# Optimization experiments

Hardware: AMD Instinct MI355X
Metric: run time of the kernel (lower is better)

Reference implementation:

```python
import jax, jax.numpy as jnp
import numpy as np

OUT_H, OUT_W = 14, 14
SPATIAL_SCALE = 0.25

def setup_inputs() -> dict:
    key = jax.random.key(0)
    k1, k2, k3, k4, k5, k6 = jax.random.split(key, 6)
    B, C, H, W = 2, 256, 200, 336
    R = 1000
    features = jax.random.normal(k1, (B, C, H, W), jnp.float32)
    img_h, img_w = H / SPATIAL_SCALE, W / SPATIAL_SCALE
    cx = jax.random.uniform(k2, (R,)) * img_w
    cy = jax.random.uniform(k3, (R,)) * img_h
    bw = jax.random.uniform(k4, (R,)) * 256.0 + 16.0
    bh = jax.random.uniform(k5, (R,)) * 256.0 + 16.0
    x1 = jnp.clip(cx - bw / 2, 0.0, img_w - 1.0)
    x2 = jnp.clip(cx + bw / 2, 0.0, img_w - 1.0)
    y1 = jnp.clip(cy - bh / 2, 0.0, img_h - 1.0)
    y2 = jnp.clip(cy + bh / 2, 0.0, img_h - 1.0)
    bidx = jax.random.randint(k6, (R,), 0, B).astype(jnp.float32)
    rois = jnp.stack([bidx, x1, y1, x2, y2], axis=1)  # (R, 5)
    return {"features": features, "rois": rois}

def _roi_align(features, rois):
    # features: (B, C, H, W); rois: (R, 5) = (batch_idx, x1, y1, x2, y2) in image coords
    B, C, H, W = features.shape
    R = rois.shape[0]
    b = jax.lax.stop_gradient(rois[:, 0]).astype(jnp.int32)
    x1, y1, x2, y2 = rois[:, 1], rois[:, 2], rois[:, 3], rois[:, 4]
    # bin-center grid in [0,1] (affine_grid identity, align_corners=False, then normalized)
    gx = (jnp.arange(OUT_W, dtype=features.dtype) + 0.5) / OUT_W
    gy = (jnp.arange(OUT_H, dtype=features.dtype) + 0.5) / OUT_H
    px = x1[:, None] + gx[None, :] * (x2 - x1)[:, None]  # (R, OUT_W) abs image x
    py = y1[:, None] + gy[None, :] * (y2 - y1)[:, None]  # (R, OUT_H) abs image y
    # grid_sample(align_corners=False) with normalized coord abs/(size/scale): pix = abs*scale - 0.5
    fx = jnp.broadcast_to(px[:, None, :], (R, OUT_H, OUT_W)) * SPATIAL_SCALE - 0.5
    fy = jnp.broadcast_to(py[:, :, None], (R, OUT_H, OUT_W)) * SPATIAL_SCALE - 0.5
    x0 = jnp.floor(fx); y0 = jnp.floor(fy)
    lx = fx - x0; ly = fy - y0
    x0i = x0.astype(jnp.int32); y0i = y0.astype(jnp.int32)
    feats_flat = features.reshape(B, C, H * W)
    bb = b[:, None, None]  # (R,1,1)
    def corner(yi, xi):
        valid = ((xi >= 0) & (xi < W) & (yi >= 0) & (yi < H)).astype(features.dtype)
        idx = jnp.clip(yi, 0, H - 1) * W + jnp.clip(xi, 0, W - 1)  # (R,OUT_H,OUT_W)
        v = feats_flat[bb, :, idx]  # (R, OUT_H, OUT_W, C)
        return v * valid[..., None]  # zeros padding_mode
    v00 = corner(y0i, x0i)
    v01 = corner(y0i, x0i + 1)
    v10 = corner(y0i + 1, x0i)
    v11 = corner(y0i + 1, x0i + 1)
    wx0 = (1.0 - lx)[..., None]; wx1 = lx[..., None]
    wy0 = (1.0 - ly)[..., None]; wy1 = ly[..., None]
    out = wy0 * (wx0 * v00 + wx1 * v01) + wy1 * (wx0 * v10 + wx1 * v11)
    return out.transpose(0, 3, 1, 2)  # (R, C, OUT_H, OUT_W)

def reference(features, rois):
    return _roi_align(features, rois)
```

## Files before the change

### kernel.cpp

```cpp
#include <hip/hip_runtime.h>

constexpr int B = 2, C = 256, H = 200, W = 336;
constexpr int HW = H * W;
constexpr int OH = 14, OW = 14, OHW = OH * OW;
constexpr float SCALE = 0.25f;
constexpr int R = 1000;

constexpr int CSPLIT = 16;
constexpr int CPB = C / CSPLIT;
constexpr int NXCD = 8;
constexpr int RPX = R / NXCD;

constexpr int NYB = 13;
constexpr int NXB = 21;
constexpr int NBUCKET = B * NYB * NXB;

typedef float f2 __attribute__((ext_vector_type(2), aligned(4)));

__global__ __launch_bounds__(1024) void bucket_rois_kernel(
    const float* __restrict__ rois, int* __restrict__ order)
{
    __shared__ int cnt[1024];
    const int t = threadIdx.x;
    cnt[t] = 0;
    __syncthreads();

    int k = 0, pos = 0;
    if (t < R) {
        const float* roi = rois + t * 5;
        const int   b  = (int)roi[0];
        const float cx = 0.5f * (roi[1] + roi[3]);
        const float cy = 0.5f * (roi[2] + roi[4]);
        const int yb = min(NYB - 1, max(0, (int)cy >> 6));
        const int xb = min(NXB - 1, max(0, (int)cx >> 6));
        k = (b * NYB + yb) * NXB + xb;
        pos = atomicAdd(&cnt[k], 1);
    }
    __syncthreads();

    for (int off = 1; off < 1024; off <<= 1) {
        const int add = (t >= off) ? cnt[t - off] : 0;
        __syncthreads();
        cnt[t] += add;
        __syncthreads();
    }

    if (t < R) {
        const int base = (k > 0) ? cnt[k - 1] : 0;
        order[base + pos] = t;
    }
}

__global__ __launch_bounds__(256, 8) void roi_align_kernel(
    const float* __restrict__ feat,
    const float* __restrict__ rois,
    const int*  __restrict__ order,
    float* __restrict__ out)
{
    const int bid   = blockIdx.x;
    const int xcd   = bid & (NXCD - 1);
    const int slot  = bid >> 3;
    const int slice = slot & (CSPLIT - 1);
    const int rank  = slot >> 4;
    const int r     = __builtin_amdgcn_readfirstlane(order[xcd * RPX + rank]);
    const int c0    = slice * CPB;
    const int s     = threadIdx.x;

    const float* roi = rois + r * 5;
    const float bf = roi[0];
    const float x1 = roi[1], y1 = roi[2], x2 = roi[3], y2 = roi[4];
    const int b = __builtin_amdgcn_readfirstlane((int)bf);

    if (s >= OHW) return;

    const int oh = s / OW;
    const int ow = s - oh * OW;

    const float fx = (x1 + (ow + 0.5f) * (1.0f / OW) * (x2 - x1)) * SCALE - 0.5f;
    const float fy = (y1 + (oh + 0.5f) * (1.0f / OH) * (y2 - y1)) * SCALE - 0.5f;

    const float x0f = floorf(fx), y0f = floorf(fy);
    const float lx = fx - x0f,   ly = fy - y0f;
    const int x0 = (int)x0f,  y0 = (int)y0f;
    const int x1i = x0 + 1,   y1i = y0 + 1;

    const float cxw0 = ((x0  >= 0 && x0  < W) ? 1.0f : 0.0f) * (1.0f - lx);
    const float cxw1 = ((x1i >= 0 && x1i < W) ? 1.0f : 0.0f) * lx;
    const float ryw0 = ((y0  >= 0 && y0  < H) ? 1.0f : 0.0f) * (1.0f - ly);
    const float ryw1 = ((y1i >= 0 && y1i < H) ? 1.0f : 0.0f) * ly;

    const int px = min(max(x0, 0), W - 2);
    const bool swp = (x0 != px);
    const float wxa = swp ? cxw1 : cxw0;
    const float wxb = swp ? cxw0 : cxw1;
    const float a0 = ryw0 * wxa, b0 = ryw0 * wxb;
    const float a1 = ryw1 * wxa, b1 = ryw1 * wxb;

    const int cy0 = min(max(y0,  0), H - 1);
    const int cy1 = min(max(y1i, 0), H - 1);
    const int i0 = cy0 * W + px;
    const int i1 = cy1 * W + px;

    const float* p  = feat + (size_t)(b * C + c0) * HW;
    float*       op = out  + (size_t)r * C * OHW + (size_t)c0 * OHW + s;

    #pragma unroll 1
    for (int cb = 0; cb < CPB; cb += 8) {
        f2 v0[8], v1[8];
        #pragma unroll
        for (int u = 0; u < 8; ++u) {
            const float* pc = p + (size_t)u * HW;
            v0[u] = *reinterpret_cast<const f2*>(pc + i0);
            v1[u] = *reinterpret_cast<const f2*>(pc + i1);
        }
        #pragma unroll
        for (int u = 0; u < 8; ++u) {
            const float v = fmaf(a0, v0[u].x,
                            fmaf(b0, v0[u].y,
                            fmaf(a1, v1[u].x, b1 * v1[u].y)));
            __builtin_nontemporal_store(v, op + u * OHW);
        }
        p  += (size_t)8 * HW;
        op += 8 * OHW;
    }
}

extern "C" void kernel_launch(void* const* d_in, const int* in_sizes, int n_in,
                              void* d_out, int out_size, void* d_ws, size_t ws_size,
                              hipStream_t stream) {
    const float* feat = (const float*)d_in[0];
    const float* rois = (const float*)d_in[1];
    float* out = (float*)d_out;
    int* order = (int*)d_ws;

    bucket_rois_kernel<<<1, 1024, 0, stream>>>(rois, order);

    dim3 grid(R * CSPLIT);
    dim3 block(256);
    roi_align_kernel<<<grid, block, 0, stream>>>(feat, rois, order, out);
}
```

Measured before the change: 387.4 us.

## Use all 256 threads by flattening channel-sample items with shared-memory coordinates

Before, only 196 of 256 threads per block did work, each looping over 16 channels. Now the first 196 threads compute sample indices and weights into LDS. After a barrier, all 256 threads process flattened (channel, sample) items in groups of 4 plus a tail, so lanes are not left idle. The cost is a block barrier, extra LDS reads, integer division per item, and fewer loads in flight per thread (4 instead of 8).

```diff
diff --git a/kernel.cpp b/kernel.cpp
--- a/kernel.cpp
+++ b/kernel.cpp
@@ -11,9 +11,10 @@
 constexpr int NXCD = 8;
 constexpr int RPX = R / NXCD;
 
+constexpr int ITEMS = CPB * OHW;
+
 constexpr int NYB = 13;
 constexpr int NXB = 21;
-constexpr int NBUCKET = B * NYB * NXB;
 
 typedef float f2 __attribute__((ext_vector_type(2), aligned(4)));
 
@@ -57,6 +58,9 @@
     const int*  __restrict__ order,
     float* __restrict__ out)
 {
+    __shared__ int   si0[OHW], si1[OHW];
+    __shared__ float sa0[OHW], sb0[OHW], sa1[OHW], sb1[OHW];
+
     const int bid   = blockIdx.x;
     const int xcd   = bid & (NXCD - 1);
     const int slot  = bid >> 3;
@@ -64,64 +68,93 @@
     const int rank  = slot >> 4;
     const int r     = __builtin_amdgcn_readfirstlane(order[xcd * RPX + rank]);
     const int c0    = slice * CPB;
-    const int s     = threadIdx.x;
+    const int tid   = threadIdx.x;
 
     const float* roi = rois + r * 5;
-    const float bf = roi[0];
     const float x1 = roi[1], y1 = roi[2], x2 = roi[3], y2 = roi[4];
-    const int b = __builtin_amdgcn_readfirstlane((int)bf);
+    const int b = __builtin_amdgcn_readfirstlane((int)roi[0]);
 
-    if (s >= OHW) return;
+    if (tid < OHW) {
+        const int oh = tid / OW;
+        const int ow = tid - oh * OW;
 
-    const int oh = s / OW;
-    const int ow = s - oh * OW;
+        const float fx = (x1 + (ow + 0.5f) * (1.0f / OW) * (x2 - x1)) * SCALE - 0.5f;
+        const float fy = (y1 + (oh + 0.5f) * (1.0f / OH) * (y2 - y1)) * SCALE - 0.5f;
 
-    const float fx = (x1 + (ow + 0.5f) * (1.0f / OW) * (x2 - x1)) * SCALE - 0.5f;
-    const float fy = (y1 + (oh + 0.5f) * (1.0f / OH) * (y2 - y1)) * SCALE - 0.5f;
+        const float x0f = floorf(fx), y0f = floorf(fy);
+        const float lx = fx - x0f,   ly = fy - y0f;
+        const int x0 = (int)x0f,  y0 = (int)y0f;
+        const int x1i = x0 + 1,   y1i = y0 + 1;
 
-    const float x0f = floorf(fx), y0f = floorf(fy);
-    const float lx = fx - x0f,   ly = fy - y0f;
-    const int x0 = (int)x0f,  y0 = (int)y0f;
-    const int x1i = x0 + 1,   y1i = y0 + 1;
+        const float cxw0 = ((x0  >= 0 && x0  < W) ? 1.0f : 0.0f) * (1.0f - lx);
+        const float cxw1 = ((x1i >= 0 && x1i < W) ? 1.0f : 0.0f) * lx;
+        const float ryw0 = ((y0  >= 0 && y0  < H) ? 1.0f : 0.0f) * (1.0f - ly);
+        const float ryw1 = ((y1i >= 0 && y1i < H) ? 1.0f : 0.0f) * ly;
 
-    const float cxw0 = ((x0  >= 0 && x0  < W) ? 1.0f : 0.0f) * (1.0f - lx);
-    const float cxw1 = ((x1i >= 0 && x1i < W) ? 1.0f : 0.0f) * lx;
-    const float ryw0 = ((y0  >= 0 && y0  < H) ? 1.0f : 0.0f) * (1.0f - ly);
-    const float ryw1 = ((y1i >= 0 && y1i < H) ? 1.0f : 0.0f) * ly;
+        const int px = min(max(x0, 0), W - 2);
+        const bool swp = (x0 != px);
+        const float wxa = swp ? cxw1 : cxw0;
+        const float wxb = swp ? cxw0 : cxw1;
 
-    const int px = min(max(x0, 0), W - 2);
-    const bool swp = (x0 != px);
-    const float wxa = swp ? cxw1 : cxw0;
-    const float wxb = swp ? cxw0 : cxw1;
-    const float a0 = ryw0 * wxa, b0 = ryw0 * wxb;
-    const float a1 = ryw1 * wxa, b1 = ryw1 * wxb;
+        const int cy0 = min(max(y0,  0), H - 1);
+        const int cy1 = min(max(y1i, 0), H - 1);
 
-    const int cy0 = min(max(y0,  0), H - 1);
-    const int cy1 = min(max(y1i, 0), H - 1);
-    const int i0 = cy0 * W + px;
-    const int i1 = cy1 * W + px;
+        si0[tid] = cy0 * W + px;
+        si1[tid] = cy1 * W + px;
+        sa0[tid] = ryw0 * wxa;
+        sb0[tid] = ryw0 * wxb;
+        sa1[tid] = ryw1 * wxa;
+        sb1[tid] = ryw1 * wxb;
+    }
+    __syncthreads();
 
     const float* p  = feat + (size_t)(b * C + c0) * HW;
-    float*       op = out  + (size_t)r * C * OHW + (size_t)c0 * OHW + s;
+    float*       ob = out  + ((size_t)r * C + c0) * OHW;
 
+    int idx = tid;
     #pragma unroll 1
-    for (int cb = 0; cb < CPB; cb += 8) {
-        f2 v0[8], v1[8];
+    for (int bb = 0; bb < 3; ++bb) {
+        const float* pa[4];
+        const float* pb[4];
+        float wa0[4], wb0[4], wa1[4], wb1[4];
+        f2 v0[4], v1[4];
+
         #pragma unroll
-        for (int u = 0; u < 8; ++u) {
-            const float* pc = p + (size_t)u * HW;
-            v0[u] = *reinterpret_cast<const f2*>(pc + i0);
-            v1[u] = *reinterpret_cast<const f2*>(pc + i1);
+        for (int u = 0; u < 4; ++u) {
+            const int id = idx + u * 256;
+            const int c  = id / OHW;
+            const int s  = id - c * OHW;
+            const int cb = c * HW;
+            pa[u] = p + cb + si0[s];
+            pb[u] = p + cb + si1[s];
+            wa0[u] = sa0[s]; wb0[u] = sb0[s];
+            wa1[u] = sa1[s]; wb1[u] = sb1[s];
         }
         #pragma unroll
-        for (int u = 0; u < 8; ++u) {
-            const float v = fmaf(a0, v0[u].x,
-                            fmaf(b0, v0[u].y,
-                            fmaf(a1, v1[u].x, b1 * v1[u].y)));
-            __builtin_nontemporal_store(v, op + u * OHW);
+        for (int u = 0; u < 4; ++u) {
+            v0[u] = *reinterpret_cast<const f2*>(pa[u]);
+            v1[u] = *reinterpret_cast<const f2*>(pb[u]);
         }
-        p  += (size_t)8 * HW;
-        op += 8 * OHW;
+        __builtin_amdgcn_sched_barrier(0);
+        #pragma unroll
+        for (int u = 0; u < 4; ++u) {
+            const float v = fmaf(wa0[u], v0[u].x,
+                            fmaf(wb0[u], v0[u].y,
+                            fmaf(wa1[u], v1[u].x, wb1[u] * v1[u].y)));
+            __builtin_nontemporal_store(v, ob + idx + u * 256);
+        }
+        idx += 1024;
+    }
+    if (idx < ITEMS) {
+        const int c  = idx / OHW;
+        const int s  = idx - c * OHW;
+        const int cb = c * HW;
+        const f2 r0 = *reinterpret_cast<const f2*>(p + cb + si0[s]);
+        const f2 r1 = *reinterpret_cast<const f2*>(p + cb + si1[s]);
+        const float v = fmaf(sa0[s], r0.x,
+                        fmaf(sb0[s], r0.y,
+                        fmaf(sa1[s], r1.x, sb1[s] * r1.y)));
+        __builtin_nontemporal_store(v, ob + idx);
     }
 }
 
```

New measurement: 383.8 us. Within noise of the previous version (-1.0%).

## Stage ROI footprint rectangle in shared memory per channel before bilinear gather

Applied to the files above, without the earlier changes.

Each block now reduces the min/max sample coordinates of its ROI, then for each channel cooperatively loads the whole covering feature rectangle into LDS and performs the bilinear interpolation from LDS instead of issuing per-thread global gathers. The intent is to turn scattered 8-byte global loads into contiguous row loads. In exchange, every channel needs two barriers, the channel loop is no longer batched 8-wide, and large ROIs load many unused pixels. The 17.7 KB LDS buffer and the dropped occupancy hint also limit the number of resident blocks.

```diff
diff --git a/kernel.cpp b/kernel.cpp
--- a/kernel.cpp
+++ b/kernel.cpp
@@ -1,4 +1,5 @@
 #include <hip/hip_runtime.h>
+#include <climits>
 
 constexpr int B = 2, C = 256, H = 200, W = 336;
 constexpr int HW = H * W;
@@ -13,9 +14,8 @@
 
 constexpr int NYB = 13;
 constexpr int NXB = 21;
-constexpr int NBUCKET = B * NYB * NXB;
 
-typedef float f2 __attribute__((ext_vector_type(2), aligned(4)));
+constexpr int RECT_ELEMS = 66 * 67;
 
 __global__ __launch_bounds__(1024) void bucket_rois_kernel(
     const float* __restrict__ rois, int* __restrict__ order)
@@ -51,12 +51,15 @@
     }
 }
 
-__global__ __launch_bounds__(256, 8) void roi_align_kernel(
+__global__ __launch_bounds__(256) void roi_align_kernel(
     const float* __restrict__ feat,
     const float* __restrict__ rois,
     const int*  __restrict__ order,
     float* __restrict__ out)
 {
+    __shared__ float rect[RECT_ELEMS];
+    __shared__ int   sred[4];
+
     const int bid   = blockIdx.x;
     const int xcd   = bid & (NXCD - 1);
     const int slot  = bid >> 3;
@@ -64,64 +67,97 @@
     const int rank  = slot >> 4;
     const int r     = __builtin_amdgcn_readfirstlane(order[xcd * RPX + rank]);
     const int c0    = slice * CPB;
-    const int s     = threadIdx.x;
+    const int tid   = threadIdx.x;
+    const int lane  = tid & 63;
 
     const float* roi = rois + r * 5;
-    const float bf = roi[0];
     const float x1 = roi[1], y1 = roi[2], x2 = roi[3], y2 = roi[4];
-    const int b = __builtin_amdgcn_readfirstlane((int)bf);
+    const int b = __builtin_amdgcn_readfirstlane((int)roi[0]);
 
-    if (s >= OHW) return;
+    int px = 0, cy0 = 0, cy1 = 0;
+    float wa0 = 0.f, wb0 = 0.f, wa1 = 0.f, wb1 = 0.f;
+    int mnpx = INT_MAX, mxpx = INT_MIN, mncy = INT_MAX, mxcy = INT_MIN;
 
-    const int oh = s / OW;
-    const int ow = s - oh * OW;
+    if (tid < OHW) {
+        const int oh = tid / OW;
+        const int ow = tid - oh * OW;
 
-    const float fx = (x1 + (ow + 0.5f) * (1.0f / OW) * (x2 - x1)) * SCALE - 0.5f;
-    const float fy = (y1 + (oh + 0.5f) * (1.0f / OH) * (y2 - y1)) * SCALE - 0.5f;
+        const float fx = (x1 + (ow + 0.5f) * (1.0f / OW) * (x2 - x1)) * SCALE - 0.5f;
+        const float fy = (y1 + (oh + 0.5f) * (1.0f / OH) * (y2 - y1)) * SCALE - 0.5f;
 
-    const float x0f = floorf(fx), y0f = floorf(fy);
-    const float lx = fx - x0f,   ly = fy - y0f;
-    const int x0 = (int)x0f,  y0 = (int)y0f;
-    const int x1i = x0 + 1,   y1i = y0 + 1;
+        const float x0f = floorf(fx), y0f = floorf(fy);
+        const float lx = fx - x0f,   ly = fy - y0f;
+        const int x0 = (int)x0f,  y0 = (int)y0f;
+        const int x1i = x0 + 1,   y1i = y0 + 1;
 
-    const float cxw0 = ((x0  >= 0 && x0  < W) ? 1.0f : 0.0f) * (1.0f - lx);
-    const float cxw1 = ((x1i >= 0 && x1i < W) ? 1.0f : 0.0f) * lx;
-    const float ryw0 = ((y0  >= 0 && y0  < H) ? 1.0f : 0.0f) * (1.0f - ly);
-    const float ryw1 = ((y1i >= 0 && y1i < H) ? 1.0f : 0.0f) * ly;
+        const float cxw0 = ((x0  >= 0 && x0  < W) ? 1.0f : 0.0f) * (1.0f - lx);
+        const float cxw1 = ((x1i >= 0 && x1i < W) ? 1.0f : 0.0f) * lx;
+        const float ryw0 = ((y0  >= 0 && y0  < H) ? 1.0f : 0.0f) * (1.0f - ly);
+        const float ryw1 = ((y1i >= 0 && y1i < H) ? 1.0f : 0.0f) * ly;
 
-    const int px = min(max(x0, 0), W - 2);
-    const bool swp = (x0 != px);
-    const float wxa = swp ? cxw1 : cxw0;
-    const float wxb = swp ? cxw0 : cxw1;
-    const float a0 = ryw0 * wxa, b0 = ryw0 * wxb;
-    const float a1 = ryw1 * wxa, b1 = ryw1 * wxb;
+        px = min(max(x0, 0), W - 2);
+        const bool swp = (x0 != px);
+        const float wxa = swp ? cxw1 : cxw0;
+        const float wxb = swp ? cxw0 : cxw1;
+        wa0 = ryw0 * wxa; wb0 = ryw0 * wxb;
+        wa1 = ryw1 * wxa; wb1 = ryw1 * wxb;
 
-    const int cy0 = min(max(y0,  0), H - 1);
-    const int cy1 = min(max(y1i, 0), H - 1);
-    const int i0 = cy0 * W + px;
-    const int i1 = cy1 * W + px;
+        cy0 = min(max(y0,  0), H - 1);
+        cy1 = min(max(y1i, 0), H - 1);
 
-    const float* p  = feat + (size_t)(b * C + c0) * HW;
-    float*       op = out  + (size_t)r * C * OHW + (size_t)c0 * OHW + s;
+        mnpx = px; mxpx = px; mncy = cy0; mxcy = cy1;
+    }
 
-    #pragma unroll 1
-    for (int cb = 0; cb < CPB; cb += 8) {
-        f2 v0[8], v1[8];
-        #pragma unroll
-        for (int u = 0; u < 8; ++u) {
-            const float* pc = p + (size_t)u * HW;
-            v0[u] = *reinterpret_cast<const f2*>(pc + i0);
-            v1[u] = *reinterpret_cast<const f2*>(pc + i1);
+    #pragma unroll
+    for (int o = 32; o; o >>= 1) {
+        mnpx = min(mnpx, __shfl_xor(mnpx, o));
+        mxpx = max(mxpx, __shfl_xor(mxpx, o));
+        mncy = min(mncy, __shfl_xor(mncy, o));
+        mxcy = max(mxcy, __shfl_xor(mxcy, o));
+    }
+    if (tid == 0) { sred[0] = INT_MAX; sred[1] = INT_MIN;
+                    sred[2] = INT_MAX; sred[3] = INT_MIN; }
+    __syncthreads();
+    if (lane == 0) {
+        atomicMin(&sred[0], mnpx); atomicMax(&sred[1], mxpx);
+        atomicMin(&sred[2], mncy); atomicMax(&sred[3], mxcy);
+    }
+    __syncthreads();
+    const int pxmin = sred[0], pxmax = sred[1];
+    const int cymin = sred[2], cymax = sred[3];
+    const int rw  = pxmax + 2 - pxmin;
+    const int rws = rw | 1;
+    const int rh  = cymax + 1 - cymin;
+    const int total = rh * rws;
+    const unsigned minv = 0xFFFFFFFFu / (unsigned)rws + 1u;
+
+    int i0 = 0, i1 = 0;
+    if (tid < OHW) {
+        i0 = (cy0 - cymin) * rws + (px - pxmin);
+        i1 = (cy1 - cymin) * rws + (px - pxmin);
+    }
+
+    const float* pc = feat + (size_t)(b * C + c0) * HW
+                           + (size_t)cymin * W + pxmin;
+    float* ob = out + ((size_t)r * C + c0) * OHW;
+
+    for (int c = 0; c < CPB; ++c) {
+        #pragma unroll 2
+        for (int i = tid; i < total; i += 256) {
+            const int row = (int)__umulhi((unsigned)i, minv);
+            const int col = i - row * rws;
+            rect[i] = pc[row * W + min(col, rw - 1)];
         }
-        #pragma unroll
-        for (int u = 0; u < 8; ++u) {
-            const float v = fmaf(a0, v0[u].x,
-                            fmaf(b0, v0[u].y,
-                            fmaf(a1, v1[u].x, b1 * v1[u].y)));
-            __builtin_nontemporal_store(v, op + u * OHW);
+        __syncthreads();
+        if (tid < OHW) {
+            const float v = fmaf(wa0, rect[i0],
+                            fmaf(wb0, rect[i0 + 1],
+                            fmaf(wa1, rect[i1], wb1 * rect[i1 + 1])));
+            __builtin_nontemporal_store(v, ob + tid);
         }
-        p  += (size_t)8 * HW;
-        op += 8 * OHW;
+        __syncthreads();
+        pc += HW;
+        ob += OHW;
     }
 }
 
```

Measured after the change: 459.9 us. +18.7%, slower.
